# Kernel optimization log

Measured on AMD Instinct MI355X. Metric: run time of the kernel, lower is better.

Reference implementation:

```python
import jax, jax.numpy as jnp
import numpy as np
import math

IN_CH, OUT_CH, K, W_DIM = 256, 256, 3, 512
B, H = 16, 128

def setup_inputs() -> dict:
    key = jax.random.key(0)
    k1, k2, k3, k4 = jax.random.split(key, 4)
    return {
        "x": jax.random.normal(k1, (B, IN_CH, H, H), dtype=jnp.float32),
        "w": jax.random.normal(k2, (B, W_DIM), dtype=jnp.float32),
        "weight": jax.random.normal(k3, (1, OUT_CH, IN_CH, K, K), dtype=jnp.float32),
        "mod_weight": jax.random.normal(k4, (IN_CH, W_DIM), dtype=jnp.float32),
        "mod_bias": jnp.zeros((IN_CH,), dtype=jnp.float32),
    }

def reference(x, w, weight, mod_weight, mod_bias):
    batch, in_ch = x.shape[0], x.shape[1]
    k = weight.shape[-1]
    pad = k // 2
    conv_scale = 1.0 / math.sqrt(in_ch * k * k)
    mod_scale = 1.0 / math.sqrt(mod_weight.shape[1])  # EqualLinear scale, lr_mul=1

    # style: [B, in_ch]
    style = w @ (mod_weight * mod_scale).T + mod_bias
    # per-sample modulated weights: [B, out_ch, in_ch, k, k]
    wt = conv_scale * weight * style[:, None, :, None, None]
    # demodulation
    d = jax.lax.rsqrt(jnp.sum(wt * wt, axis=(2, 3, 4), keepdims=True) + 1e-8)
    wt = wt * d

    def conv_one(xi, wi):
        # xi: [in_ch, H, W], wi: [out_ch, in_ch, k, k]
        return jax.lax.conv_general_dilated(
            xi[None], wi, window_strides=(1, 1),
            padding=[(pad, pad), (pad, pad)],
            dimension_numbers=("NCHW", "OIHW", "NCHW"))[0]

    # [B, out_ch, H, W]
    return jax.vmap(conv_one)(x, wt)
```

## Files before the change

kernel.cpp:

```cpp
#include <hip/hip_runtime.h>
#include <math.h>

#define IN_CH  256
#define OUT_CH 256
#define WDIM   512
#define BATCH  16
#define HH     128

typedef _Float16 f16;
typedef f16   f16x8 __attribute__((ext_vector_type(8)));
typedef float f32x4 __attribute__((ext_vector_type(4)));

#define NCOL 130

__device__ __host__ inline size_t wblock(int b, int dydx, int ocg, int chunk) {
    return ((((size_t)b * 9 + dydx) * 2 + ocg) * 8 + chunk) * 4096;
}

__global__ void style_kernel(const float* __restrict__ w,
                             const float* __restrict__ mod_weight,
                             const float* __restrict__ mod_bias,
                             float* __restrict__ style) {
    const int b = blockIdx.x;
    const int i = threadIdx.x;
    __shared__ float wsh[WDIM];
    for (int j = threadIdx.x; j < WDIM; j += 256) wsh[j] = w[b * WDIM + j];
    __syncthreads();
    const float mod_scale = 1.0f / sqrtf((float)WDIM);
    float acc = 0.f;
    const float* mwp = mod_weight + (size_t)i * WDIM;
    for (int j = 0; j < WDIM; ++j) acc += wsh[j] * mwp[j];
    style[b * IN_CH + i] = acc * mod_scale + mod_bias[i];
}

__global__ void demod_kernel(const float* __restrict__ weight,
                             const float* __restrict__ style,
                             float* __restrict__ dfac) {
    const int b = blockIdx.x;
    const int o = threadIdx.x;
    __shared__ float s2[IN_CH];
    for (int j = threadIdx.x; j < IN_CH; j += 256) {
        float s = style[b * IN_CH + j];
        s2[j] = s * s;
    }
    __syncthreads();
    const float conv_scale2 = 1.0f / 2304.0f;
    float acc = 0.f;
    const float* wp = weight + (size_t)o * IN_CH * 9;
    for (int i = 0; i < IN_CH; ++i) {
        float sq = 0.f;
#pragma unroll
        for (int r = 0; r < 9; ++r) { float v = wp[i * 9 + r]; sq += v * v; }
        acc += sq * s2[i];
    }
    dfac[b * OUT_CH + o] = rsqrtf(acc * conv_scale2 + 1e-8f);
}

__global__ void wmod_kernel(const float* __restrict__ weight,
                            const float* __restrict__ style,
                            const float* __restrict__ dfac,
                            f16* __restrict__ wmod) {
    const int oc = blockIdx.x;
    const int b  = blockIdx.y;
    const int ic = threadIdx.x;
    const float sd = style[b * IN_CH + ic] * (1.0f / 48.0f) * dfac[b * OUT_CH + oc];
    const float* wp = weight + ((size_t)oc * IN_CH + ic) * 9;
    const int ocg = oc >> 7, ocl = oc & 127;
    const int chunk = ic >> 5, icl = ic & 31;
#pragma unroll
    for (int r = 0; r < 9; ++r) {
        f16 h = (f16)(wp[r] * sd);
        wmod[wblock(b, r, ocg, chunk) + (size_t)ocl * 32 + icl] = h;
    }
}

__global__ __launch_bounds__(256, 3) void conv_mfma(
        const float* __restrict__ x,
        const f16*  __restrict__ wmod,
        float* __restrict__ out) {
    __shared__ uint4 xs4[3 * NCOL * 4];
    __shared__ uint4 wls4[2][512];

    const int y0  = blockIdx.x;
    const int ocg = blockIdx.y;
    const int b   = blockIdx.z;

    const int t  = threadIdx.x;
    const int l  = t & 63;
    const int w  = t >> 6;
    const int wm = w >> 1, wn = w & 1;
    const int lm = l & 15, lg = l >> 4;

    f32x4 acc[4][4];
#pragma unroll
    for (int i = 0; i < 4; ++i)
#pragma unroll
        for (int j = 0; j < 4; ++j) acc[i][j] = (f32x4){0.f, 0.f, 0.f, 0.f};

    if (t < 24) {
        int blk = t >> 2;
        int r = blk >> 1;
        int c = (blk & 1) ? 129 : 0;
        uint4 z = {0u, 0u, 0u, 0u};
        xs4[(r * NCOL + c) * 4 + (t & 3)] = z;
    }

    const int cq = t & 31;
    const int gq = t >> 5;

    auto stageX = [&](int chunk) {
        const int ic0 = chunk * 32;
#pragma unroll
        for (int r = 0; r < 3; ++r) {
            const int gy = y0 - 1 + r;
            float vv[4][4];
            if (gy >= 0 && gy < HH) {
#pragma unroll
                for (int rr = 0; rr < 4; ++rr) {
                    const float* gp = x + (((size_t)(b * IN_CH + ic0 + 4 * gq + rr)) * HH + gy) * HH + 4 * cq;
                    float4 q = *(const float4*)gp;
                    vv[rr][0] = q.x; vv[rr][1] = q.y; vv[rr][2] = q.z; vv[rr][3] = q.w;
                }
            } else {
#pragma unroll
                for (int rr = 0; rr < 4; ++rr)
#pragma unroll
                    for (int cc = 0; cc < 4; ++cc) vv[rr][cc] = 0.f;
            }
#pragma unroll
            for (int cc = 0; cc < 4; ++cc) {
                const int c = 1 + 4 * cq + cc;
                const int lsel = ((gq >> 1) + (c >> 2)) & 3;
                union { f16 h[4]; uint2 u2; } pk;
                pk.h[0] = (f16)vv[0][cc]; pk.h[1] = (f16)vv[1][cc];
                pk.h[2] = (f16)vv[2][cc]; pk.h[3] = (f16)vv[3][cc];
                char* p = (char*)xs4 + (((size_t)r * NCOL + c) << 6) + (lsel << 4) + ((gq & 1) << 3);
                *(uint2*)p = pk.u2;
            }
        }
    };

    {
        const uint4* g = (const uint4*)(wmod + wblock(b, 0, ocg, 0));
        wls4[0][t]       = g[t];
        wls4[0][t + 256] = g[t + 256];
    }
    stageX(0);
    __syncthreads();

    int cur = 0;
    for (int chunk = 0; chunk < 8; ++chunk) {
        for (int dydx = 0; dydx < 9; ++dydx) {
            const bool hasnext = !(chunk == 7 && dydx == 8);
            int nd = dydx + 1, nb = chunk;
            if (nd == 9) { nd = 0; nb = chunk + 1; }
            uint4 p0, p1;
            if (hasnext) {
                const uint4* g = (const uint4*)(wmod + wblock(b, nd, ocg, nb));
                p0 = g[t]; p1 = g[t + 256];
            }

            const int dy = dydx / 3;
            const int dx = dydx - 3 * dy;

            f16x8 af[4];
#pragma unroll
            for (int mt = 0; mt < 4; ++mt) {
                const int ocl = wm * 64 + mt * 16 + lm;
                const char* ap = (const char*)wls4[cur] + ((size_t)ocl << 6) + (lg << 4);
                af[mt] = *(const f16x8*)ap;
            }
#pragma unroll
            for (int nt = 0; nt < 4; ++nt) {
                const int c = wn * 64 + nt * 16 + lm + dx;
                const int lsel = (lg + (c >> 2)) & 3;
                const char* bp = (const char*)xs4 + (((size_t)dy * NCOL + c) << 6) + (lsel << 4);
                f16x8 bf = *(const f16x8*)bp;
#pragma unroll
                for (int mt = 0; mt < 4; ++mt) {
                    acc[mt][nt] = __builtin_amdgcn_mfma_f32_16x16x32_f16(af[mt], bf, acc[mt][nt], 0, 0, 0);
                }
            }

            if (hasnext) {
                uint4* d = wls4[cur ^ 1];
                d[t] = p0; d[t + 256] = p1;
            }
            __syncthreads();
            cur ^= 1;
        }
        if (chunk < 7) {
            stageX(chunk + 1);
            __syncthreads();
        }
    }

#pragma unroll
    for (int mt = 0; mt < 4; ++mt) {
#pragma unroll
        for (int nt = 0; nt < 4; ++nt) {
            const int col = wn * 64 + nt * 16 + lm;
#pragma unroll
            for (int reg = 0; reg < 4; ++reg) {
                const int oc = ocg * 128 + wm * 64 + mt * 16 + lg * 4 + reg;
                out[(((size_t)(b * OUT_CH + oc)) * HH + y0) * HH + col] = acc[mt][nt][reg];
            }
        }
    }
}

#define TILE_H 32
#define TILE_W 64
#define OCB    8
#define ICH    4
#define XS_COLS 66
#define XS_STRIDE 68
#define XS_ROWS 34

__global__ __launch_bounds__(256, 3) void conv_kernel(
        const float* __restrict__ x,
        const float* __restrict__ weight,
        const float* __restrict__ style,
        const float* __restrict__ dfac,
        float* __restrict__ out) {
    __shared__ float xs[ICH][XS_ROWS * XS_STRIDE];
    __shared__ float wmod[ICH][OCB][12];

    const int tile = blockIdx.x;
    const int ocg  = blockIdx.y;
    const int b    = blockIdx.z;
    const int y0 = (tile >> 1) * TILE_H;
    const int x0 = (tile & 1) * TILE_W;

    const int t  = threadIdx.x;
    const int ty = t >> 3;
    const int tx = t & 7;

    const float conv_scale = 1.0f / 48.0f;

    float acc[OCB][8];
#pragma unroll
    for (int o = 0; o < OCB; ++o)
#pragma unroll
        for (int j = 0; j < 8; ++j) acc[o][j] = 0.f;

    const float* xb = x + (size_t)b * IN_CH * HH * HH;
    const float* stb = style + b * IN_CH;
    const float* dfb = dfac + b * OUT_CH;

    for (int ic0 = 0; ic0 < IN_CH; ic0 += ICH) {
        __syncthreads();
        for (int icl = 0; icl < ICH; ++icl) {
            const float* xc = xb + (size_t)(ic0 + icl) * HH * HH;
            for (int s = t; s < XS_ROWS * XS_COLS; s += 256) {
                int row = s / XS_COLS;
                int col = s - row * XS_COLS;
                int gy = y0 + row - 1;
                int gx = x0 + col - 1;
                float v = 0.f;
                if (gy >= 0 && gy < HH && gx >= 0 && gx < HH) v = xc[gy * HH + gx];
                xs[icl][row * XS_STRIDE + col] = v;
            }
        }
        for (int s = t; s < ICH * OCB * 9; s += 256) {
            int icl = s / (OCB * 9);
            int rem = s - icl * (OCB * 9);
            int o   = rem / 9;
            int r   = rem - o * 9;
            int oc  = ocg * OCB + o;
            int ic  = ic0 + icl;
            float wv = weight[((size_t)oc * IN_CH + ic) * 9 + r];
            wmod[icl][o][r] = wv * (conv_scale * stb[ic] * dfb[oc]);
        }
        __syncthreads();
#pragma unroll 1
        for (int icl = 0; icl < ICH; ++icl) {
            float xr[3][10];
#pragma unroll
            for (int dy = 0; dy < 3; ++dy) {
                const float* p = &xs[icl][(ty + dy) * XS_STRIDE + 8 * tx];
                float4 a  = *(const float4*)(p);
                float4 bv = *(const float4*)(p + 4);
                float2 c  = *(const float2*)(p + 8);
                xr[dy][0] = a.x;  xr[dy][1] = a.y;  xr[dy][2] = a.z;  xr[dy][3] = a.w;
                xr[dy][4] = bv.x; xr[dy][5] = bv.y; xr[dy][6] = bv.z; xr[dy][7] = bv.w;
                xr[dy][8] = c.x;  xr[dy][9] = c.y;
            }
#pragma unroll
            for (int o = 0; o < OCB; ++o) {
                const float* wp = wmod[icl][o];
                float w0 = wp[0], w1 = wp[1], w2 = wp[2];
                float w3 = wp[3], w4 = wp[4], w5 = wp[5];
                float w6 = wp[6], w7 = wp[7], w8 = wp[8];
#pragma unroll
                for (int j = 0; j < 8; ++j) {
                    acc[o][j] += w0 * xr[0][j]     + w1 * xr[0][j + 1] + w2 * xr[0][j + 2]
                               + w3 * xr[1][j]     + w4 * xr[1][j + 1] + w5 * xr[1][j + 2]
                               + w6 * xr[2][j]     + w7 * xr[2][j + 1] + w8 * xr[2][j + 2];
                }
            }
        }
    }

    const int gy = y0 + ty;
    const int gx = x0 + 8 * tx;
#pragma unroll
    for (int o = 0; o < OCB; ++o) {
        int oc = ocg * OCB + o;
        float* op = out + (((size_t)b * OUT_CH + oc) * HH + gy) * HH + gx;
        float4 v0 = {acc[o][0], acc[o][1], acc[o][2], acc[o][3]};
        float4 v1 = {acc[o][4], acc[o][5], acc[o][6], acc[o][7]};
        *(float4*)(op)     = v0;
        *(float4*)(op + 4) = v1;
    }
}

extern "C" void kernel_launch(void* const* d_in, const int* in_sizes, int n_in,
                              void* d_out, int out_size, void* d_ws, size_t ws_size,
                              hipStream_t stream) {
    const float* x          = (const float*)d_in[0];
    const float* w          = (const float*)d_in[1];
    const float* weight     = (const float*)d_in[2];
    const float* mod_weight = (const float*)d_in[3];
    const float* mod_bias   = (const float*)d_in[4];
    float* out = (float*)d_out;

    float* style = (float*)d_ws;
    float* dfac  = style + BATCH * IN_CH;

    style_kernel<<<dim3(BATCH), dim3(256), 0, stream>>>(w, mod_weight, mod_bias, style);
    demod_kernel<<<dim3(BATCH), dim3(256), 0, stream>>>(weight, style, dfac);

    const size_t need = 32768 + (size_t)BATCH * 9 * 2 * 8 * 4096 * sizeof(f16);
    if (ws_size >= need) {
        f16* wmodp = (f16*)((char*)d_ws + 32768);
        wmod_kernel<<<dim3(256, BATCH), dim3(256), 0, stream>>>(weight, style, dfac, wmodp);
        conv_mfma<<<dim3(128, 2, BATCH), dim3(256), 0, stream>>>(x, wmodp, out);
    } else {
        conv_kernel<<<dim3(8, 32, BATCH), dim3(256), 0, stream>>>(x, weight, style, dfac, out);
    }
}
```

Baseline: 833.8 us.

## Restructure conv pipeline: register A-fragments, double-buffered X tiles, swizzled grid, parallel prep

```diff
diff --git a/kernel.cpp b/kernel.cpp
--- a/kernel.cpp
+++ b/kernel.cpp
@@ -12,6 +12,7 @@
 typedef float f32x4 __attribute__((ext_vector_type(4)));
 
 #define NCOL 130
+#define XSLOTS (3 * NCOL * 4)
 
 __device__ __host__ inline size_t wblock(int b, int dydx, int ocg, int chunk) {
     return ((((size_t)b * 9 + dydx) * 2 + ocg) * 8 + chunk) * 4096;
@@ -21,56 +22,64 @@
                              const float* __restrict__ mod_weight,
                              const float* __restrict__ mod_bias,
                              float* __restrict__ style) {
-    const int b = blockIdx.x;
-    const int i = threadIdx.x;
-    __shared__ float wsh[WDIM];
-    for (int j = threadIdx.x; j < WDIM; j += 256) wsh[j] = w[b * WDIM + j];
-    __syncthreads();
-    const float mod_scale = 1.0f / sqrtf((float)WDIM);
+    const int b = blockIdx.y;
+    const int i = blockIdx.x * 64 + threadIdx.x;
+    const float4* wp = (const float4*)(w + (size_t)b * WDIM);
+    const float4* mp = (const float4*)(mod_weight + (size_t)i * WDIM);
     float acc = 0.f;
-    const float* mwp = mod_weight + (size_t)i * WDIM;
-    for (int j = 0; j < WDIM; ++j) acc += wsh[j] * mwp[j];
-    style[b * IN_CH + i] = acc * mod_scale + mod_bias[i];
-}
-
-__global__ void demod_kernel(const float* __restrict__ weight,
+#pragma unroll 8
+    for (int j = 0; j < WDIM / 4; ++j) {
+        float4 a = wp[j], c = mp[j];
+        acc += a.x * c.x + a.y * c.y + a.z * c.z + a.w * c.w;
+    }
+    style[b * IN_CH + i] = acc * (1.0f / sqrtf((float)WDIM)) + mod_bias[i];
+}
+
+__global__ void wsq_kernel(const float* __restrict__ weight,
+                           float* __restrict__ q) {
+    const int o = blockIdx.x, i = threadIdx.x;
+    const float* wp = weight + ((size_t)o * IN_CH + i) * 9;
+    float s = 0.f;
+#pragma unroll
+    for (int r = 0; r < 9; ++r) { float v = wp[r]; s += v * v; }
+    q[o * IN_CH + i] = s;
+}
+
+__global__ void demod_kernel(const float* __restrict__ q,
                              const float* __restrict__ style,
                              float* __restrict__ dfac) {
-    const int b = blockIdx.x;
-    const int o = threadIdx.x;
-    __shared__ float s2[IN_CH];
-    for (int j = threadIdx.x; j < IN_CH; j += 256) {
-        float s = style[b * IN_CH + j];
-        s2[j] = s * s;
-    }
-    __syncthreads();
-    const float conv_scale2 = 1.0f / 2304.0f;
-    float acc = 0.f;
-    const float* wp = weight + (size_t)o * IN_CH * 9;
-    for (int i = 0; i < IN_CH; ++i) {
-        float sq = 0.f;
-#pragma unroll
-        for (int r = 0; r < 9; ++r) { float v = wp[i * 9 + r]; sq += v * v; }
-        acc += sq * s2[i];
-    }
-    dfac[b * OUT_CH + o] = rsqrtf(acc * conv_scale2 + 1e-8f);
+    const int o = blockIdx.x, b = blockIdx.y, t = threadIdx.x;
+    float4 qv = *(const float4*)(q + (size_t)o * IN_CH + 4 * t);
+    float4 sv = *(const float4*)(style + (size_t)b * IN_CH + 4 * t);
+    float s = qv.x * sv.x * sv.x + qv.y * sv.y * sv.y
+            + qv.z * sv.z * sv.z + qv.w * sv.w * sv.w;
+#pragma unroll
+    for (int off = 32; off > 0; off >>= 1) s += __shfl_down(s, off, 64);
+    if (t == 0) dfac[b * OUT_CH + o] = rsqrtf(s * (1.0f / 2304.0f) + 1e-8f);
 }
 
 __global__ void wmod_kernel(const float* __restrict__ weight,
                             const float* __restrict__ style,
                             const float* __restrict__ dfac,
                             f16* __restrict__ wmod) {
-    const int oc = blockIdx.x;
-    const int b  = blockIdx.y;
-    const int ic = threadIdx.x;
-    const float sd = style[b * IN_CH + ic] * (1.0f / 48.0f) * dfac[b * OUT_CH + oc];
-    const float* wp = weight + ((size_t)oc * IN_CH + ic) * 9;
-    const int ocg = oc >> 7, ocl = oc & 127;
-    const int chunk = ic >> 5, icl = ic & 31;
-#pragma unroll
-    for (int r = 0; r < 9; ++r) {
-        f16 h = (f16)(wp[r] * sd);
-        wmod[wblock(b, r, ocg, chunk) + (size_t)ocl * 32 + icl] = h;
+    const int r = blockIdx.x, ocg = blockIdx.y, b = blockIdx.z;
+    const int t = threadIdx.x;
+    const int ocl = t >> 1, half = t & 1;
+    const int oc = ocg * 128 + ocl;
+    const float sd = dfac[b * OUT_CH + oc] * (1.0f / 48.0f);
+    const float* wp = weight + (size_t)oc * IN_CH * 9 + r;
+    const float* sp = style + (size_t)b * IN_CH;
+    for (int chunk = 0; chunk < 8; ++chunk) {
+        const int icb = chunk * 32 + half * 16;
+        union { f16 h[16]; uint4 u[2]; } buf;
+#pragma unroll
+        for (int j = 0; j < 16; ++j) {
+            const int ic = icb + j;
+            buf.h[j] = (f16)(wp[(size_t)ic * 9] * sp[ic] * sd);
+        }
+        uint4* dst = (uint4*)(wmod + wblock(b, r, ocg, chunk) + (size_t)ocl * 32 + half * 16);
+        dst[0] = buf.u[0];
+        dst[1] = buf.u[1];
     }
 }
 
@@ -78,12 +87,13 @@
         const float* __restrict__ x,
         const f16*  __restrict__ wmod,
         float* __restrict__ out) {
-    __shared__ uint4 xs4[3 * NCOL * 4];
-    __shared__ uint4 wls4[2][512];
-
-    const int y0  = blockIdx.x;
-    const int ocg = blockIdx.y;
-    const int b   = blockIdx.z;
+    __shared__ uint4 xs4[2 * XSLOTS];
+
+    const int bid = blockIdx.x;
+    const int lid = (bid & 7) * 512 + (bid >> 3);
+    const int ocg = lid & 1;
+    const int y0  = (lid >> 1) & 127;
+    const int b   = lid >> 8;
 
     const int t  = threadIdx.x;
     const int l  = t & 63;
@@ -97,19 +107,21 @@
 #pragma unroll
         for (int j = 0; j < 4; ++j) acc[i][j] = (f32x4){0.f, 0.f, 0.f, 0.f};
 
-    if (t < 24) {
-        int blk = t >> 2;
+    if (t < 48) {
+        int buf = t / 24, rem = t - 24 * buf;
+        int blk = rem >> 2;
         int r = blk >> 1;
         int c = (blk & 1) ? 129 : 0;
         uint4 z = {0u, 0u, 0u, 0u};
-        xs4[(r * NCOL + c) * 4 + (t & 3)] = z;
+        xs4[buf * XSLOTS + (r * NCOL + c) * 4 + (rem & 3)] = z;
     }
 
     const int cq = t & 31;
     const int gq = t >> 5;
 
-    auto stageX = [&](int chunk) {
+    auto stageX = [&](int chunk, int buf) {
         const int ic0 = chunk * 32;
+        uint4* xbuf = xs4 + buf * XSLOTS;
 #pragma unroll
         for (int r = 0; r < 3; ++r) {
             const int gy = y0 - 1 + r;
@@ -118,8 +130,8 @@
 #pragma unroll
                 for (int rr = 0; rr < 4; ++rr) {
                     const float* gp = x + (((size_t)(b * IN_CH + ic0 + 4 * gq + rr)) * HH + gy) * HH + 4 * cq;
-                    float4 q = *(const float4*)gp;
-                    vv[rr][0] = q.x; vv[rr][1] = q.y; vv[rr][2] = q.z; vv[rr][3] = q.w;
+                    float4 qv = *(const float4*)gp;
+                    vv[rr][0] = qv.x; vv[rr][1] = qv.y; vv[rr][2] = qv.z; vv[rr][3] = qv.w;
                 }
             } else {
 #pragma unroll
@@ -134,65 +146,54 @@
                 union { f16 h[4]; uint2 u2; } pk;
                 pk.h[0] = (f16)vv[0][cc]; pk.h[1] = (f16)vv[1][cc];
                 pk.h[2] = (f16)vv[2][cc]; pk.h[3] = (f16)vv[3][cc];
-                char* p = (char*)xs4 + (((size_t)r * NCOL + c) << 6) + (lsel << 4) + ((gq & 1) << 3);
+                char* p = (char*)xbuf + (((size_t)r * NCOL + c) << 6) + (lsel << 4) + ((gq & 1) << 3);
                 *(uint2*)p = pk.u2;
             }
         }
     };
 
-    {
-        const uint4* g = (const uint4*)(wmod + wblock(b, 0, ocg, 0));
-        wls4[0][t]       = g[t];
-        wls4[0][t + 256] = g[t + 256];
-    }
-    stageX(0);
+    auto aload = [&](int chunk, int dydx, f16x8* dst) {
+        const f16* p = wmod + wblock(b, dydx, ocg, chunk);
+#pragma unroll
+        for (int mt = 0; mt < 4; ++mt) {
+            const int ocl = wm * 64 + mt * 16 + lm;
+            dst[mt] = *(const f16x8*)(p + (size_t)ocl * 32 + lg * 8);
+        }
+    };
+
+    f16x8 afc[4], afn[4];
+    aload(0, 0, afc);
+    stageX(0, 0);
     __syncthreads();
 
     int cur = 0;
     for (int chunk = 0; chunk < 8; ++chunk) {
+        if (chunk < 7) stageX(chunk + 1, cur ^ 1);
+        const uint4* xbuf = xs4 + cur * XSLOTS;
+#pragma unroll
         for (int dydx = 0; dydx < 9; ++dydx) {
-            const bool hasnext = !(chunk == 7 && dydx == 8);
             int nd = dydx + 1, nb = chunk;
             if (nd == 9) { nd = 0; nb = chunk + 1; }
-            uint4 p0, p1;
-            if (hasnext) {
-                const uint4* g = (const uint4*)(wmod + wblock(b, nd, ocg, nb));
-                p0 = g[t]; p1 = g[t + 256];
-            }
+            if (nb < 8) aload(nb, nd, afn);
 
             const int dy = dydx / 3;
             const int dx = dydx - 3 * dy;
-
-            f16x8 af[4];
-#pragma unroll
-            for (int mt = 0; mt < 4; ++mt) {
-                const int ocl = wm * 64 + mt * 16 + lm;
-                const char* ap = (const char*)wls4[cur] + ((size_t)ocl << 6) + (lg << 4);
-                af[mt] = *(const f16x8*)ap;
-            }
 #pragma unroll
             for (int nt = 0; nt < 4; ++nt) {
                 const int c = wn * 64 + nt * 16 + lm + dx;
                 const int lsel = (lg + (c >> 2)) & 3;
-                const char* bp = (const char*)xs4 + (((size_t)dy * NCOL + c) << 6) + (lsel << 4);
+                const char* bp = (const char*)xbuf + (((size_t)dy * NCOL + c) << 6) + (lsel << 4);
                 f16x8 bf = *(const f16x8*)bp;
 #pragma unroll
                 for (int mt = 0; mt < 4; ++mt) {
-                    acc[mt][nt] = __builtin_amdgcn_mfma_f32_16x16x32_f16(af[mt], bf, acc[mt][nt], 0, 0, 0);
+                    acc[mt][nt] = __builtin_amdgcn_mfma_f32_16x16x32_f16(afc[mt], bf, acc[mt][nt], 0, 0, 0);
                 }
             }
-
-            if (hasnext) {
-                uint4* d = wls4[cur ^ 1];
-                d[t] = p0; d[t + 256] = p1;
-            }
-            __syncthreads();
-            cur ^= 1;
-        }
-        if (chunk < 7) {
-            stageX(chunk + 1);
-            __syncthreads();
-        }
+#pragma unroll
+            for (int mt = 0; mt < 4; ++mt) afc[mt] = afn[mt];
+        }
+        __syncthreads();
+        cur ^= 1;
     }
 
 #pragma unroll
@@ -217,6 +218,28 @@
 #define XS_STRIDE 68
 #define XS_ROWS 34
 
+__global__ void demod_fb_kernel(const float* __restrict__ weight,
+                                const float* __restrict__ style,
+                                float* __restrict__ dfac) {
+    const int b = blockIdx.x;
+    const int o = threadIdx.x;
+    __shared__ float s2[IN_CH];
+    for (int j = threadIdx.x; j < IN_CH; j += 256) {
+        float s = style[b * IN_CH + j];
+        s2[j] = s * s;
+    }
+    __syncthreads();
+    float acc2 = 0.f;
+    const float* wp = weight + (size_t)o * IN_CH * 9;
+    for (int i = 0; i < IN_CH; ++i) {
+        float sq = 0.f;
+#pragma unroll
+        for (int r = 0; r < 9; ++r) { float v = wp[i * 9 + r]; sq += v * v; }
+        acc2 += sq * s2[i];
+    }
+    dfac[b * OUT_CH + o] = rsqrtf(acc2 * (1.0f / 2304.0f) + 1e-8f);
+}
+
 __global__ __launch_bounds__(256, 3) void conv_kernel(
         const float* __restrict__ x,
         const float* __restrict__ weight,
@@ -224,7 +247,7 @@
         const float* __restrict__ dfac,
         float* __restrict__ out) {
     __shared__ float xs[ICH][XS_ROWS * XS_STRIDE];
-    __shared__ float wmod[ICH][OCB][12];
+    __shared__ float wsm[ICH][OCB][12];
 
     const int tile = blockIdx.x;
     const int ocg  = blockIdx.y;
@@ -235,8 +258,6 @@
     const int t  = threadIdx.x;
     const int ty = t >> 3;
     const int tx = t & 7;
-
-    const float conv_scale = 1.0f / 48.0f;
 
     float acc[OCB][8];
 #pragma unroll
@@ -270,7 +291,7 @@
             int oc  = ocg * OCB + o;
             int ic  = ic0 + icl;
             float wv = weight[((size_t)oc * IN_CH + ic) * 9 + r];
-            wmod[icl][o][r] = wv * (conv_scale * stb[ic] * dfb[oc]);
+            wsm[icl][o][r] = wv * ((1.0f / 48.0f) * stb[ic] * dfb[oc]);
         }
         __syncthreads();
 #pragma unroll 1
@@ -288,7 +309,7 @@
             }
 #pragma unroll
             for (int o = 0; o < OCB; ++o) {
-                const float* wp = wmod[icl][o];
+                const float* wp = wsm[icl][o];
                 float w0 = wp[0], w1 = wp[1], w2 = wp[2];
                 float w3 = wp[3], w4 = wp[4], w5 = wp[5];
                 float w6 = wp[6], w7 = wp[7], w8 = wp[8];
@@ -327,16 +348,21 @@
 
     float* style = (float*)d_ws;
     float* dfac  = style + BATCH * IN_CH;
-
-    style_kernel<<<dim3(BATCH), dim3(256), 0, stream>>>(w, mod_weight, mod_bias, style);
-    demod_kernel<<<dim3(BATCH), dim3(256), 0, stream>>>(weight, style, dfac);
-
-    const size_t need = 32768 + (size_t)BATCH * 9 * 2 * 8 * 4096 * sizeof(f16);
+    float* q     = dfac + BATCH * OUT_CH;
+    f16*   wmodp = (f16*)((char*)d_ws + 16384 + 16384 + 262144);
+
+    const size_t need = 16384 + 16384 + 262144
+                      + (size_t)BATCH * 9 * 2 * 8 * 4096 * sizeof(f16);
+
+    style_kernel<<<dim3(4, BATCH), dim3(64), 0, stream>>>(w, mod_weight, mod_bias, style);
+
     if (ws_size >= need) {
-        f16* wmodp = (f16*)((char*)d_ws + 32768);
-        wmod_kernel<<<dim3(256, BATCH), dim3(256), 0, stream>>>(weight, style, dfac, wmodp);
-        conv_mfma<<<dim3(128, 2, BATCH), dim3(256), 0, stream>>>(x, wmodp, out);
+        wsq_kernel<<<dim3(256), dim3(256), 0, stream>>>(weight, q);
+        demod_kernel<<<dim3(256, BATCH), dim3(64), 0, stream>>>(q, style, dfac);
+        wmod_kernel<<<dim3(9, 2, BATCH), dim3(256), 0, stream>>>(weight, style, dfac, wmodp);
+        conv_mfma<<<dim3(4096), dim3(256), 0, stream>>>(x, wmodp, out);
     } else {
+        demod_fb_kernel<<<dim3(BATCH), dim3(256), 0, stream>>>(weight, style, dfac);
         conv_kernel<<<dim3(8, 32, BATCH), dim3(256), 0, stream>>>(x, weight, style, dfac, out);
     }
 }
```

New measurement: 778.4 us. -6.6%, faster.
